# Kernel optimization log

Measured on AMD Instinct MI355X. Metric: run time of the kernel, lower is better.

Reference implementation:

```python
import jax, jax.numpy as jnp
import numpy as np

B, L, D, H = 2, 4096, 1024, 8
DK = D // H   # per-head key dim = 128
DV = D // H   # per-head value dim = 128
K_CONV = 4
CHUNK = 64
EPS = 1e-6


def _rmsnorm(x, w):
    return x * jax.lax.rsqrt(jnp.mean(x * x, axis=-1, keepdims=True) + EPS) * w


def _l2norm(x):
    return x * jax.lax.rsqrt(jnp.sum(x * x, axis=-1, keepdims=True) + EPS)


def _short_conv(x, w):
    # causal depthwise conv (FLA ShortConvolution) + silu. x: [B,L,C], w: [C,K]
    Kc = w.shape[-1]
    Ln = x.shape[1]
    xp = jnp.pad(x, ((0, 0), (Kc - 1, 0), (0, 0)))
    y = xp[:, 0:Ln, :] * w[:, 0]
    for i in range(1, Kc):
        y = y + xp[:, i:i + Ln, :] * w[:, i]
    return jax.nn.silu(y)


def _delta_chunkwise(q, k, v, beta, chunk=CHUNK):
    # q,k: [B,H,L,DK], v: [B,H,L,DV], beta: [B,H,L]
    Bb, Hh, Ll, Dk = q.shape
    Dv = v.shape[-1]
    q = q * (Dk ** -0.5)
    nC = Ll // chunk  # L divisible by chunk here, no padding needed
    qc = q.reshape(Bb, Hh, nC, chunk, Dk).transpose(2, 0, 1, 3, 4)
    kc = k.reshape(Bb, Hh, nC, chunk, Dk).transpose(2, 0, 1, 3, 4)
    vc = v.reshape(Bb, Hh, nC, chunk, Dv).transpose(2, 0, 1, 3, 4)
    bc = beta.reshape(Bb, Hh, nC, chunk).transpose(2, 0, 1, 3)
    eye = jnp.eye(chunk, dtype=q.dtype)
    causal = jnp.tril(jnp.ones((chunk, chunk), dtype=q.dtype))

    def step(S, inp):
        q_c, k_c, v_c, b_c = inp
        kk = jnp.einsum('bhik,bhjk->bhij', k_c, k_c)
        A = eye + jnp.tril(b_c[..., :, None] * kk, k=-1)
        A_inv = jax.lax.linalg.triangular_solve(
            A, jnp.broadcast_to(eye, A.shape), left_side=True, lower=True,
            transpose_a=False, conjugate_a=False, unit_diagonal=False)
        w_ = jnp.einsum('bhij,bhjk->bhik', A_inv, k_c * b_c[..., None])
        u_ = jnp.einsum('bhij,bhjv->bhiv', A_inv, v_c * b_c[..., None])
        v_new = u_ - jnp.einsum('bhik,bhkv->bhiv', w_, S)
        qk = jnp.einsum('bhik,bhjk->bhij', q_c, k_c)
        o = jnp.einsum('bhik,bhkv->bhiv', q_c, S) + jnp.einsum('bhij,bhjv->bhiv', qk * causal, v_new)
        S_new = S + jnp.einsum('bhik,bhiv->bhkv', k_c, v_new)
        return S_new, o

    S0 = jnp.zeros((Bb, Hh, Dk, Dv), dtype=q.dtype)
    S_f, outs = jax.lax.scan(step, S0, (qc, kc, vc, bc))
    out = outs.transpose(1, 2, 0, 3, 4).reshape(Bb, Hh, Ll, Dv)
    return out, S_f


def setup_inputs() -> dict:
    key = jax.random.key(0)
    ks = jax.random.split(key, 9)
    s = 0.02
    return {
        'x': jax.random.normal(ks[0], (B, L, D), jnp.float32),
        'norm_w': jnp.ones((D,), jnp.float32),
        'Wq': jax.random.normal(ks[1], (D, D), jnp.float32) * s,
        'Wk': jax.random.normal(ks[2], (D, D), jnp.float32) * s,
        'Wv': jax.random.normal(ks[3], (D, D), jnp.float32) * s,
        'Wb': jax.random.normal(ks[4], (D, H), jnp.float32) * s,
        'conv_q': jax.random.normal(ks[5], (D, K_CONV), jnp.float32) * 0.3,
        'conv_k': jax.random.normal(ks[6], (D, K_CONV), jnp.float32) * 0.3,
        'conv_v': jax.random.normal(ks[7], (D, K_CONV), jnp.float32) * 0.3,
        'o_norm_w': jnp.ones((DV,), jnp.float32),
        'Wo': jax.random.normal(ks[8], (D, D), jnp.float32) * s,
    }


def reference(x, norm_w, Wq, Wk, Wv, Wb, conv_q, conv_k, conv_v, o_norm_w, Wo):
    h = _rmsnorm(x, norm_w)
    q = _short_conv(h @ Wq, conv_q)
    k = _short_conv(h @ Wk, conv_k)
    v = _short_conv(h @ Wv, conv_v)
    beta = jax.nn.sigmoid(h @ Wb)                      # [B,L,H]
    qh = q.reshape(B, L, H, DK).transpose(0, 2, 1, 3)  # [B,H,L,DK]
    kh = k.reshape(B, L, H, DK).transpose(0, 2, 1, 3)
    vh = v.reshape(B, L, H, DV).transpose(0, 2, 1, 3)
    qh = _l2norm(jax.nn.silu(qh))  # qk_activation=silu, qk_norm=l2
    kh = _l2norm(jax.nn.silu(kh))
    bh = beta.transpose(0, 2, 1)   # [B,H,L]
    o, _ = _delta_chunkwise(qh, kh, vh, bh)
    o = o.transpose(0, 2, 1, 3)    # [B,L,H,DV]
    o = _rmsnorm(o, o_norm_w)      # per-head output RMSNorm
    return x + o.reshape(B, L, D) @ Wo
```

## Files before the change

kernel.cpp:

```cpp
#include <hip/hip_runtime.h>
#include <hip/hip_bf16.h>

#define B_ 2
#define L_ 4096
#define D_ 1024
#define H_ 8
#define DK_ 128
#define NR_ (B_*L_)
#define NC_ 64
#define CS_ 64

typedef __attribute__((ext_vector_type(8))) short short8;
typedef __attribute__((ext_vector_type(4))) float f32x4;

__device__ __forceinline__ float sigmf(float x){ return 1.0f/(1.0f+__expf(-x)); }
__device__ __forceinline__ float siluf(float x){ return x/(1.0f+__expf(-x)); }
__device__ __forceinline__ unsigned short f2bf(float f){
  __hip_bfloat16 h = __float2bfloat16(f);
  return *reinterpret_cast<unsigned short*>(&h);
}
__device__ __forceinline__ void gll16(const void* g, void* l){
  __builtin_amdgcn_global_load_lds((const __attribute__((address_space(1))) void*)g,
      (__attribute__((address_space(3))) void*)l, 16, 0, 0);
}

__global__ __launch_bounds__(256) void rmsnorm_kernel(const float* __restrict__ x,
    const float* __restrict__ w, float* __restrict__ h, unsigned short* __restrict__ hb){
  int n = blockIdx.x; int t = threadIdx.x;
  float4 v = ((const float4*)(x + (size_t)n*D_))[t];
  float ss = v.x*v.x + v.y*v.y + v.z*v.z + v.w*v.w;
  #pragma unroll
  for (int m=32;m>0;m>>=1) ss += __shfl_xor(ss, m, 64);
  __shared__ float red[4];
  if ((t&63)==0) red[t>>6] = ss;
  __syncthreads();
  ss = red[0]+red[1]+red[2]+red[3];
  float rs = rsqrtf(ss*(1.0f/D_) + 1e-6f);
  float4 wv = ((const float4*)w)[t];
  float4 o; o.x=v.x*rs*wv.x; o.y=v.y*rs*wv.y; o.z=v.z*rs*wv.z; o.w=v.w*rs*wv.w;
  ((float4*)(h + (size_t)n*D_))[t] = o;
  ushort4 ob4; ob4.x=f2bf(o.x); ob4.y=f2bf(o.y); ob4.z=f2bf(o.z); ob4.w=f2bf(o.w);
  ((ushort4*)(hb + (size_t)n*D_))[t] = ob4;
}

__global__ __launch_bounds__(256) void transpose_bf16_kernel(const float* __restrict__ W,
    unsigned short* __restrict__ Wt){
  __shared__ float tile[64][65];
  int bi = blockIdx.y, bj = blockIdx.x;
  int tx = threadIdx.x & 63, tg = threadIdx.x >> 6;
  #pragma unroll
  for (int i=0;i<16;i++){
    int r = tg*16 + i;
    tile[r][tx] = W[(size_t)(bi*64 + r)*D_ + bj*64 + tx];
  }
  __syncthreads();
  #pragma unroll
  for (int i=0;i<16;i++){
    int r = tg*16 + i;
    Wt[(size_t)(bj*64 + r)*D_ + bi*64 + tx] = f2bf(tile[tx][r]);
  }
}

__global__ __launch_bounds__(256) void gemm_bf16(const unsigned short* __restrict__ A,
    const unsigned short* __restrict__ Bt, const float* __restrict__ R,
    float* __restrict__ C, int N, int K){
  __shared__ __align__(16) unsigned short Al[4096];
  __shared__ __align__(16) unsigned short Bl[4096];
  int t = threadIdx.x, w = t>>6, l = t&63;
  int wm = w&1, wn = w>>1;
  int row0 = blockIdx.y*128, col0 = blockIdx.x*128;
  int lr = l&15, lk = l>>4;
  const unsigned short* ga0 = A  + (size_t)(row0 + w*16     + lr)*K + lk*8;
  const unsigned short* ga1 = A  + (size_t)(row0 + (w+4)*16 + lr)*K + lk*8;
  const unsigned short* gb0 = Bt + (size_t)(col0 + w*16     + lr)*K + lk*8;
  const unsigned short* gb1 = Bt + (size_t)(col0 + (w+4)*16 + lr)*K + lk*8;
  unsigned short* la0 = &Al[(w*64 + l)*8];
  unsigned short* la1 = &Al[((w+4)*64 + l)*8];
  unsigned short* lb0 = &Bl[(w*64 + l)*8];
  unsigned short* lb1 = &Bl[((w+4)*64 + l)*8];
  f32x4 acc[4][4];
  #pragma unroll
  for (int i=0;i<4;i++)
    #pragma unroll
    for (int j=0;j<4;j++) acc[i][j] = (f32x4){0.f,0.f,0.f,0.f};
  for (int k0=0;k0<K;k0+=32){
    gll16(ga0 + k0, la0);
    gll16(ga1 + k0, la1);
    gll16(gb0 + k0, lb0);
    gll16(gb1 + k0, lb1);
    __syncthreads();
    short8 af[4], bfr[4];
    #pragma unroll
    for (int i=0;i<4;i++) af[i]  = *(const short8*)&Al[((wm*4+i)*64 + l)*8];
    #pragma unroll
    for (int j=0;j<4;j++) bfr[j] = *(const short8*)&Bl[((wn*4+j)*64 + l)*8];
    #pragma unroll
    for (int i=0;i<4;i++)
      #pragma unroll
      for (int j=0;j<4;j++)
        acc[i][j] = __builtin_amdgcn_mfma_f32_16x16x32_bf16(af[i], bfr[j], acc[i][j], 0,0,0);
    __syncthreads();
  }
  int orow = row0 + wm*64 + (l>>4)*4;
  int ocol = col0 + wn*64 + (l&15);
  #pragma unroll
  for (int i=0;i<4;i++){
    #pragma unroll
    for (int j=0;j<4;j++){
      #pragma unroll
      for (int r=0;r<4;r++){
        size_t idx = (size_t)(orow + i*16 + r)*N + ocol + j*16;
        float res = R ? R[idx] : 0.0f;
        C[idx] = acc[i][j][r] + res;
      }
    }
  }
}

__global__ __launch_bounds__(256) void beta_kernel(const float* __restrict__ h,
    const float* __restrict__ Wb, float* __restrict__ beta){
  int n = blockIdx.x, t = threadIdx.x;
  const float* hr = h + (size_t)n*D_;
  float p[8] = {};
  for (int kx=t; kx<D_; kx+=256){
    float hv = hr[kx];
    const float* wr = Wb + (size_t)kx*H_;
    #pragma unroll
    for (int j=0;j<8;j++) p[j] += hv*wr[j];
  }
  #pragma unroll
  for (int m=32;m>0;m>>=1){
    #pragma unroll
    for (int j=0;j<8;j++) p[j] += __shfl_xor(p[j], m, 64);
  }
  __shared__ float red[4][8];
  if ((t&63)==0){
    #pragma unroll
    for (int j=0;j<8;j++) red[t>>6][j] = p[j];
  }
  __syncthreads();
  if (t < 8){
    float s = red[0][t]+red[1][t]+red[2][t]+red[3][t];
    beta[(size_t)n*H_ + t] = sigmf(s);
  }
}

__global__ __launch_bounds__(256) void conv_silu_kernel(const float* __restrict__ in,
    const float* __restrict__ w, float* __restrict__ out, int ld){
  size_t idx = (size_t)blockIdx.x*256 + threadIdx.x;
  int c = (int)(idx & (D_-1));
  int n = (int)(idx >> 10);
  int l = n & (L_-1);
  const float* src = in + (size_t)n*ld + c;
  float4 wv = ((const float4*)w)[c];
  float acc = wv.w * src[0];
  if (l >= 1) acc += wv.z * src[-ld];
  if (l >= 2) acc += wv.y * src[-2*ld];
  if (l >= 3) acc += wv.x * src[-3*ld];
  out[(size_t)n*D_ + c] = siluf(acc);
}

__global__ __launch_bounds__(256) void silu_l2norm_kernel(float* __restrict__ a, float scale,
    unsigned short* __restrict__ ob){
  int n = blockIdx.x, t = threadIdx.x;
  float* row = a + (size_t)n*D_;
  float4 v = ((const float4*)row)[t];
  float4 u; u.x=siluf(v.x); u.y=siluf(v.y); u.z=siluf(v.z); u.w=siluf(v.w);
  float ss = u.x*u.x+u.y*u.y+u.z*u.z+u.w*u.w;
  #pragma unroll
  for (int m=16;m>0;m>>=1) ss += __shfl_xor(ss, m, 64);
  float rs = rsqrtf(ss + 1e-6f) * scale;
  u.x*=rs; u.y*=rs; u.z*=rs; u.w*=rs;
  ((float4*)row)[t] = u;
  if (ob){
    ushort4 r4; r4.x=f2bf(u.x); r4.y=f2bf(u.y); r4.z=f2bf(u.z); r4.w=f2bf(u.w);
    ((ushort4*)(ob + (size_t)n*D_))[t] = r4;
  }
}

__global__ __launch_bounds__(256) void chunk_local_kernel(
    const float* __restrict__ q, const float* __restrict__ k, const float* __restrict__ v,
    const float* __restrict__ beta, unsigned short* __restrict__ wneg_buf,
    float* __restrict__ u_buf, unsigned short* __restrict__ qk_buf,
    unsigned short* __restrict__ kt_buf){
  int ci = blockIdx.x, bh = blockIdx.y;
  int b = bh >> 3, hh = bh & 7;
  int n0 = b*L_ + ci*CS_;
  int cbase = hh*DK_;
  int cid = bh*NC_ + ci;
  __shared__ float Ks[64][132];
  __shared__ float Als[64*68];
  __shared__ float rowW[144];
  __shared__ float rowU[144];
  __shared__ float bs[64];
  int t = threadIdx.x;
  {
    int r = t >> 2, c0 = (t & 3)*32;
    const float* kr = k + (size_t)(n0+r)*D_ + cbase + c0;
    #pragma unroll
    for (int m=0;m<32;m+=4) *(float4*)&Ks[r][c0+m] = *(const float4*)&kr[m];
  }
  if (t < 64) bs[t] = beta[(size_t)(n0+t)*H_ + hh];
  __syncthreads();
  int ti = t >> 4, tj = t & 15;
  {
    float cc[4][4] = {};
    #pragma unroll 2
    for (int d=0; d<128; d+=4){
      float4 ar[4], br[4];
      #pragma unroll
      for (int r2=0;r2<4;r2++) ar[r2] = *(const float4*)&Ks[ti+16*r2][d];
      #pragma unroll
      for (int s2=0;s2<4;s2++) br[s2] = *(const float4*)&Ks[tj+16*s2][d];
      #pragma unroll
      for (int r2=0;r2<4;r2++){
        #pragma unroll
        for (int s2=0;s2<4;s2++){
          cc[r2][s2] += ar[r2].x*br[s2].x + ar[r2].y*br[s2].y
                      + ar[r2].z*br[s2].z + ar[r2].w*br[s2].w;
        }
      }
    }
    #pragma unroll
    for (int r2=0;r2<4;r2++){
      #pragma unroll
      for (int s2=0;s2<4;s2++){
        int i2 = ti + 16*r2, j2 = tj + 16*s2;
        Als[i2*68 + j2] = (j2 < i2) ? bs[i2]*cc[r2][s2] : 0.0f;
      }
    }
  }
  __syncthreads();
  int i = t >> 2, part = t & 3, ds = part*32, dp = part*36;
  float wreg[32], ureg[32];
  {
    float bi = bs[i];
    const float* vr = v + (size_t)(n0+i)*D_ + cbase + ds;
    #pragma unroll
    for (int m=0;m<32;m++) wreg[m] = bi * Ks[i][ds+m];
    #pragma unroll
    for (int m=0;m<32;m+=4){
      float4 vv = *(const float4*)&vr[m];
      ureg[m+0]=bi*vv.x; ureg[m+1]=bi*vv.y; ureg[m+2]=bi*vv.z; ureg[m+3]=bi*vv.w;
    }
  }
  for (int j=0;j<63;j++){
    if (i == j){
      #pragma unroll
      for (int m=0;m<32;m++){ rowW[dp+m]=wreg[m]; rowU[dp+m]=ureg[m]; }
    }
    __syncthreads();
    if (i > j){
      float aj = Als[i*68 + j];
      #pragma unroll
      for (int m=0;m<32;m++){ wreg[m] -= aj*rowW[dp+m]; ureg[m] -= aj*rowU[dp+m]; }
    }
    __syncthreads();
  }
  {
    unsigned short* wd = wneg_buf + (size_t)cid*(64*128) + (size_t)i*128 + ds;
    float* ud = u_buf + (size_t)cid*(64*128) + (size_t)i*128 + ds;
    #pragma unroll
    for (int m=0;m<32;m+=4){
      ushort4 f; f.x=f2bf(-wreg[m]); f.y=f2bf(-wreg[m+1]); f.z=f2bf(-wreg[m+2]); f.w=f2bf(-wreg[m+3]);
      *(ushort4*)&wd[m] = f;
      float4 g; g.x=ureg[m]; g.y=ureg[m+1]; g.z=ureg[m+2]; g.w=ureg[m+3];
      *(float4*)&ud[m] = g;
    }
  }
  __syncthreads();
  {
    const float* qbase = q + (size_t)n0*D_ + cbase;
    float cc[4][4] = {};
    #pragma unroll 2
    for (int d=0; d<128; d+=4){
      float4 ar[4], br[4];
      #pragma unroll
      for (int r2=0;r2<4;r2++) ar[r2] = *(const float4*)&qbase[(size_t)(ti+16*r2)*D_ + d];
      #pragma unroll
      for (int s2=0;s2<4;s2++) br[s2] = *(const float4*)&Ks[tj+16*s2][d];
      #pragma unroll
      for (int r2=0;r2<4;r2++){
        #pragma unroll
        for (int s2=0;s2<4;s2++){
          cc[r2][s2] += ar[r2].x*br[s2].x + ar[r2].y*br[s2].y
                      + ar[r2].z*br[s2].z + ar[r2].w*br[s2].w;
        }
      }
    }
    unsigned short* qkd = qk_buf + (size_t)cid*4096;
    #pragma unroll
    for (int r2=0;r2<4;r2++){
      #pragma unroll
      for (int s2=0;s2<4;s2++){
        int i2 = ti+16*r2, j2 = tj+16*s2;
        qkd[i2*64 + j2] = (j2 <= i2) ? f2bf(cc[r2][s2]) : (unsigned short)0;
      }
    }
  }
  {
    unsigned short* ktd = kt_buf + (size_t)cid*(64*128);
    for (int idx = t; idx < 8192; idx += 256){
      int d = idx >> 6, i2 = idx & 63;
      ktd[idx] = f2bf(Ks[i2][d]);
    }
  }
}

__global__ __launch_bounds__(256) void seq_kernel(
    const unsigned short* __restrict__ wneg_buf, const float* __restrict__ u_buf,
    const unsigned short* __restrict__ kt_buf, const unsigned short* __restrict__ qk_buf,
    const unsigned short* __restrict__ qbh, float* __restrict__ o_buf){
  int bid = blockIdx.x;
  int bh = bid & 15, cg = bid >> 4;
  int b = bh >> 3, hh = bh & 7;
  int cbase = hh*DK_;
  int t = threadIdx.x;
  int wv = t >> 6, l = t & 63, g = l >> 4, lr = l & 15;

  __shared__ __align__(16) unsigned short Wl[2][8192];
  __shared__ __align__(16) unsigned short Ql[2][8192];
  __shared__ __align__(16) unsigned short Ktl[2][8192];
  __shared__ __align__(16) unsigned short qkl[2][4096];
  __shared__ __align__(16) float  Ul[2][2048];
  __shared__ __align__(16) unsigned short Stl[32*136];
  __shared__ __align__(16) unsigned short vTl[32*72];

  f32x4 Sacc[2][2];
  #pragma unroll
  for (int mc=0;mc<2;mc++)
    #pragma unroll
    for (int ntl=0;ntl<2;ntl++) Sacc[mc][ntl] = (f32x4){0.f,0.f,0.f,0.f};

  for (int z=t; z<32*136; z+=256) Stl[z] = 0;
  __syncthreads();

  size_t cid0 = (size_t)bh*NC_;
  const unsigned short* wb_  = wneg_buf + cid0*8192;
  const unsigned short* ktb_ = kt_buf  + cid0*8192;
  const unsigned short* qkb_ = qk_buf  + cid0*4096;
  const float*          ub_  = u_buf   + cid0*8192;
  const unsigned short* qb_  = qbh + (size_t)(b*L_)*D_ + cbase;

  int hv = wv >> 1, lv = wv & 1;

  #define STAGE(BI, CI) do { \
    const unsigned short* wp  = wb_  + (size_t)(CI)*8192; \
    const unsigned short* kp  = ktb_ + (size_t)(CI)*8192; \
    const unsigned short* qkp = qkb_ + (size_t)(CI)*4096; \
    const float*          up  = ub_  + (size_t)(CI)*8192; \
    const unsigned short* qp  = qb_  + (size_t)(CI)*CS_*D_; \
    _Pragma("unroll") \
    for (int r=0;r<4;r++){ \
      gll16(wp + (size_t)(16*r + lr)*128 + wv*32 + g*8, &Wl[BI][(r*4+wv)*512 + l*8]); \
      gll16(qp + (size_t)(16*r + lr)*D_  + wv*32 + g*8, &Ql[BI][(r*4+wv)*512 + l*8]); \
      int fn = 2*r + hv; \
      gll16(kp + (size_t)(16*fn + lr)*64 + lv*32 + g*8, &Ktl[BI][(r*4+wv)*512 + l*8]); \
    } \
    _Pragma("unroll") \
    for (int r=0;r<2;r++){ \
      int fm = 2*r + hv; \
      gll16(qkp + (size_t)(16*fm + lr)*64 + lv*32 + g*8, &qkl[BI][(r*4+wv)*512 + l*8]); \
      int idx = r*256 + t; \
      gll16(up + (size_t)(idx>>3)*128 + cg*32 + (idx&7)*4, &Ul[BI][idx*4]); \
    } \
  } while(0)

  STAGE(0, 0);
  asm volatile("s_waitcnt vmcnt(0)" ::: "memory");
  __builtin_amdgcn_s_barrier();
  __builtin_amdgcn_sched_barrier(0);

  int cur = 0;
  for (int ci=0; ci<NC_; ++ci){
    int cn = (ci+1 < NC_) ? ci+1 : ci;
    STAGE(cur^1, cn);

    f32x4 accV[2];
    #pragma unroll
    for (int nt=0;nt<2;nt++){
      #pragma unroll
      for (int r=0;r<4;r++) accV[nt][r] = Ul[cur][(16*wv + 4*g + r)*32 + 16*nt + lr];
    }
    #pragma unroll
    for (int kq=0;kq<4;kq++){
      short8 a  = *(const short8*)&Wl[cur][(wv*4+kq)*512 + l*8];
      short8 b0 = *(const short8*)&Stl[(0  + lr)*136 + kq*32 + g*8];
      short8 b1 = *(const short8*)&Stl[(16 + lr)*136 + kq*32 + g*8];
      accV[0] = __builtin_amdgcn_mfma_f32_16x16x32_bf16(a, b0, accV[0], 0,0,0);
      accV[1] = __builtin_amdgcn_mfma_f32_16x16x32_bf16(a, b1, accV[1], 0,0,0);
    }
    #pragma unroll
    for (int nt=0;nt<2;nt++){
      #pragma unroll
      for (int r=0;r<4;r++)
        vTl[(16*nt + lr)*72 + 16*wv + 4*g + r] = f2bf(accV[nt][r]);
    }
    asm volatile("s_waitcnt lgkmcnt(0)" ::: "memory");
    __builtin_amdgcn_s_barrier();
    __builtin_amdgcn_sched_barrier(0);

    f32x4 accO[2];
    accO[0] = (f32x4){0.f,0.f,0.f,0.f}; accO[1] = (f32x4){0.f,0.f,0.f,0.f};
    #pragma unroll
    for (int kq=0;kq<4;kq++){
      short8 a  = *(const short8*)&Ql[cur][(wv*4+kq)*512 + l*8];
      short8 b0 = *(const short8*)&Stl[(0  + lr)*136 + kq*32 + g*8];
      short8 b1 = *(const short8*)&Stl[(16 + lr)*136 + kq*32 + g*8];
      accO[0] = __builtin_amdgcn_mfma_f32_16x16x32_bf16(a, b0, accO[0], 0,0,0);
      accO[1] = __builtin_amdgcn_mfma_f32_16x16x32_bf16(a, b1, accO[1], 0,0,0);
    }
    #pragma unroll
    for (int kq=0;kq<2;kq++){
      short8 a  = *(const short8*)&qkl[cur][(wv*2+kq)*512 + l*8];
      short8 b0 = *(const short8*)&vTl[(0  + lr)*72 + kq*32 + g*8];
      short8 b1 = *(const short8*)&vTl[(16 + lr)*72 + kq*32 + g*8];
      accO[0] = __builtin_amdgcn_mfma_f32_16x16x32_bf16(a, b0, accO[0], 0,0,0);
      accO[1] = __builtin_amdgcn_mfma_f32_16x16x32_bf16(a, b1, accO[1], 0,0,0);
    }
    {
      int n0 = b*L_ + ci*CS_;
      #pragma unroll
      for (int nt=0;nt<2;nt++){
        #pragma unroll
        for (int r=0;r<4;r++)
          o_buf[(size_t)(n0 + 16*wv + 4*g + r)*D_ + cbase + cg*32 + 16*nt + lr] = accO[nt][r];
      }
    }
    asm volatile("s_waitcnt lgkmcnt(0)" ::: "memory");
    __builtin_amdgcn_s_barrier();
    __builtin_amdgcn_sched_barrier(0);

    #pragma unroll
    for (int kq=0;kq<2;kq++){
      short8 a0 = *(const short8*)&vTl[(0  + lr)*72 + kq*32 + g*8];
      short8 a1 = *(const short8*)&vTl[(16 + lr)*72 + kq*32 + g*8];
      short8 b0 = *(const short8*)&Ktl[cur][((2*wv+0)*2 + kq)*512 + l*8];
      short8 b1 = *(const short8*)&Ktl[cur][((2*wv+1)*2 + kq)*512 + l*8];
      Sacc[0][0] = __builtin_amdgcn_mfma_f32_16x16x32_bf16(a0, b0, Sacc[0][0], 0,0,0);
      Sacc[0][1] = __builtin_amdgcn_mfma_f32_16x16x32_bf16(a0, b1, Sacc[0][1], 0,0,0);
      Sacc[1][0] = __builtin_amdgcn_mfma_f32_16x16x32_bf16(a1, b0, Sacc[1][0], 0,0,0);
      Sacc[1][1] = __builtin_amdgcn_mfma_f32_16x16x32_bf16(a1, b1, Sacc[1][1], 0,0,0);
    }
    #pragma unroll
    for (int mc=0;mc<2;mc++){
      #pragma unroll
      for (int ntl=0;ntl<2;ntl++){
        #pragma unroll
        for (int r=0;r<4;r++)
          Stl[(16*mc + 4*g + r)*136 + 32*wv + 16*ntl + lr] = f2bf(Sacc[mc][ntl][r]);
      }
    }
    asm volatile("s_waitcnt lgkmcnt(0)" ::: "memory");
    asm volatile("s_waitcnt vmcnt(4)" ::: "memory");
    __builtin_amdgcn_s_barrier();
    __builtin_amdgcn_sched_barrier(0);
    cur ^= 1;
  }
  #undef STAGE
}

__global__ __launch_bounds__(256) void head_rmsnorm_kernel(const float* __restrict__ o,
    const float* __restrict__ w, unsigned short* __restrict__ out){
  int n = blockIdx.x, t = threadIdx.x;
  float4 v = ((const float4*)(o + (size_t)n*D_))[t];
  float ss = v.x*v.x+v.y*v.y+v.z*v.z+v.w*v.w;
  #pragma unroll
  for (int m=16;m>0;m>>=1) ss += __shfl_xor(ss, m, 64);
  float rs = rsqrtf(ss*(1.0f/DK_) + 1e-6f);
  float4 wv = ((const float4*)w)[t & 31];
  float4 u; u.x=v.x*rs*wv.x; u.y=v.y*rs*wv.y; u.z=v.z*rs*wv.z; u.w=v.w*rs*wv.w;
  ushort4 r4; r4.x=f2bf(u.x); r4.y=f2bf(u.y); r4.z=f2bf(u.z); r4.w=f2bf(u.w);
  ((ushort4*)(out + (size_t)n*D_))[t] = r4;
}

extern "C" void kernel_launch(void* const* d_in, const int* in_sizes, int n_in,
                              void* d_out, int out_size, void* d_ws, size_t ws_size,
                              hipStream_t stream){
  const float* x      = (const float*)d_in[0];
  const float* norm_w = (const float*)d_in[1];
  const float* Wq     = (const float*)d_in[2];
  const float* Wk     = (const float*)d_in[3];
  const float* Wv     = (const float*)d_in[4];
  const float* Wb     = (const float*)d_in[5];
  const float* conv_q = (const float*)d_in[6];
  const float* conv_k = (const float*)d_in[7];
  const float* conv_v = (const float*)d_in[8];
  const float* onw    = (const float*)d_in[9];
  const float* Wo     = (const float*)d_in[10];
  float* out = (float*)d_out;

  const size_t NB = (size_t)NR_*D_;
  float* ws   = (float*)d_ws;
  float* h    = ws;
  float* qkv  = ws + NB;
  float* qb   = ws + 4*NB;
  float* kb   = ws + 5*NB;
  float* vb   = ws + 6*NB;
  float* betab= ws + 7*NB;
  unsigned short* wtq = (unsigned short*)(betab + 65536);
  unsigned short* wtk = wtq + (size_t)D_*D_;
  unsigned short* wtv = wtk + (size_t)D_*D_;
  unsigned short* wto = wtv + (size_t)D_*D_;
  unsigned short* hb  = (unsigned short*)qb;
  unsigned short* obb = (unsigned short*)h;
  unsigned short* wneg = (unsigned short*)qkv;
  unsigned short* ktb  = wneg + (size_t)8*1024*1024;
  unsigned short* qkbf = ktb  + (size_t)8*1024*1024;
  unsigned short* qbh  = qkbf + (size_t)4*1024*1024;
  float*          ubuf = (float*)(qbh + (size_t)8*1024*1024);

  rmsnorm_kernel<<<NR_, 256, 0, stream>>>(x, norm_w, h, hb);
  dim3 tg(16,16);
  transpose_bf16_kernel<<<tg, 256, 0, stream>>>(Wq, wtq);
  transpose_bf16_kernel<<<tg, 256, 0, stream>>>(Wk, wtk);
  transpose_bf16_kernel<<<tg, 256, 0, stream>>>(Wv, wtv);
  transpose_bf16_kernel<<<tg, 256, 0, stream>>>(Wo, wto);
  dim3 gq(3*D_/128, NR_/128);
  gemm_bf16<<<gq, 256, 0, stream>>>(hb, wtq, nullptr, qkv, 3*D_, D_);
  beta_kernel<<<NR_, 256, 0, stream>>>(h, Wb, betab);
  conv_silu_kernel<<<(int)(NB/256), 256, 0, stream>>>(qkv,        conv_q, qb, 3*D_);
  conv_silu_kernel<<<(int)(NB/256), 256, 0, stream>>>(qkv + D_,   conv_k, kb, 3*D_);
  conv_silu_kernel<<<(int)(NB/256), 256, 0, stream>>>(qkv + 2*D_, conv_v, vb, 3*D_);
  const float qscale = 0.08838834764831845f;
  silu_l2norm_kernel<<<NR_, 256, 0, stream>>>(qb, qscale, qbh);
  silu_l2norm_kernel<<<NR_, 256, 0, stream>>>(kb, 1.0f, nullptr);
  chunk_local_kernel<<<dim3(NC_, 16), 256, 0, stream>>>(qb, kb, vb, betab,
      wneg, ubuf, qkbf, ktb);
  seq_kernel<<<64, 256, 0, stream>>>(wneg, ubuf, ktb, qkbf, qbh, vb);
  head_rmsnorm_kernel<<<NR_, 256, 0, stream>>>(vb, onw, obb);
  dim3 gg(D_/128, NR_/128);
  gemm_bf16<<<gg, 256, 0, stream>>>(obb, wto, x, out, D_, D_);
  (void)in_sizes; (void)n_in; (void)out_size; (void)ws_size;
}
```

Before: 744.2 us.

## Fuse conv+silu+l2norm for q/k and restructure seq kernel to 512 threads

Merges the causal depthwise conv+silu with the silu+l2norm pass for q and k into one row kernel, so the intermediate q/k buffers are not written and reread. The sequential chunk kernel goes from 256 to 512 threads, with each wave owning one 16x16 output tile. The state update is overlapped with the output computation by double-buffering the bf16 state in LDS, which removes one barrier per chunk. The bf16 q buffer is moved into a workspace region no longer in use, and the layout of the staged loads is recomputed once up front.

New measurement: 688.6 us. 7.5% less time.

```diff
diff --git a/kernel.cpp b/kernel.cpp
--- a/kernel.cpp
+++ b/kernel.cpp
@@ -160,18 +160,33 @@
   out[(size_t)n*D_ + c] = siluf(acc);
 }
 
-__global__ __launch_bounds__(256) void silu_l2norm_kernel(float* __restrict__ a, float scale,
-    unsigned short* __restrict__ ob){
+__global__ __launch_bounds__(256) void conv_silu_l2norm_kernel(const float* __restrict__ in,
+    const float* __restrict__ w, float* __restrict__ outf, unsigned short* __restrict__ ob,
+    float scale, int ld){
   int n = blockIdx.x, t = threadIdx.x;
-  float* row = a + (size_t)n*D_;
-  float4 v = ((const float4*)row)[t];
-  float4 u; u.x=siluf(v.x); u.y=siluf(v.y); u.z=siluf(v.z); u.w=siluf(v.w);
+  int c0 = t*4;
+  int l = n & (L_-1);
+  const float* src = in + (size_t)n*ld + c0;
+  float4 x0 = *(const float4*)&src[0];
+  float4 x1 = (l>=1) ? *(const float4*)&src[-ld]   : (float4){0,0,0,0};
+  float4 x2 = (l>=2) ? *(const float4*)&src[-2*ld] : (float4){0,0,0,0};
+  float4 x3 = (l>=3) ? *(const float4*)&src[-3*ld] : (float4){0,0,0,0};
+  float4 w0 = ((const float4*)w)[c0+0];
+  float4 w1 = ((const float4*)w)[c0+1];
+  float4 w2 = ((const float4*)w)[c0+2];
+  float4 w3 = ((const float4*)w)[c0+3];
+  float4 u;
+  u.x = siluf(w0.w*x0.x + w0.z*x1.x + w0.y*x2.x + w0.x*x3.x);
+  u.y = siluf(w1.w*x0.y + w1.z*x1.y + w1.y*x2.y + w1.x*x3.y);
+  u.z = siluf(w2.w*x0.z + w2.z*x1.z + w2.y*x2.z + w2.x*x3.z);
+  u.w = siluf(w3.w*x0.w + w3.z*x1.w + w3.y*x2.w + w3.x*x3.w);
+  u.x = siluf(u.x); u.y = siluf(u.y); u.z = siluf(u.z); u.w = siluf(u.w);
   float ss = u.x*u.x+u.y*u.y+u.z*u.z+u.w*u.w;
   #pragma unroll
   for (int m=16;m>0;m>>=1) ss += __shfl_xor(ss, m, 64);
   float rs = rsqrtf(ss + 1e-6f) * scale;
   u.x*=rs; u.y*=rs; u.z*=rs; u.w*=rs;
-  ((float4*)row)[t] = u;
+  ((float4*)(outf + (size_t)n*D_))[t] = u;
   if (ob){
     ushort4 r4; r4.x=f2bf(u.x); r4.y=f2bf(u.y); r4.z=f2bf(u.z); r4.w=f2bf(u.w);
     ((ushort4*)(ob + (size_t)n*D_))[t] = r4;
@@ -307,7 +322,7 @@
   }
 }
 
-__global__ __launch_bounds__(256) void seq_kernel(
+__global__ __launch_bounds__(512) void seq_kernel(
     const unsigned short* __restrict__ wneg_buf, const float* __restrict__ u_buf,
     const unsigned short* __restrict__ kt_buf, const unsigned short* __restrict__ qk_buf,
     const unsigned short* __restrict__ qbh, float* __restrict__ o_buf){
@@ -316,24 +331,23 @@
   int b = bh >> 3, hh = bh & 7;
   int cbase = hh*DK_;
   int t = threadIdx.x;
-  int wv = t >> 6, l = t & 63, g = l >> 4, lr = l & 15;
+  int w = t >> 6, l = t & 63, g = l >> 4, lr = l & 15;
+  int mt = w >> 1, nt = w & 1;
+  int ct = w >> 2, dtp = (w & 3)*2;
 
   __shared__ __align__(16) unsigned short Wl[2][8192];
   __shared__ __align__(16) unsigned short Ql[2][8192];
   __shared__ __align__(16) unsigned short Ktl[2][8192];
   __shared__ __align__(16) unsigned short qkl[2][4096];
   __shared__ __align__(16) float  Ul[2][2048];
-  __shared__ __align__(16) unsigned short Stl[32*136];
+  __shared__ __align__(16) unsigned short Stl[2][32*136];
   __shared__ __align__(16) unsigned short vTl[32*72];
 
-  f32x4 Sacc[2][2];
-  #pragma unroll
-  for (int mc=0;mc<2;mc++)
-    #pragma unroll
-    for (int ntl=0;ntl<2;ntl++) Sacc[mc][ntl] = (f32x4){0.f,0.f,0.f,0.f};
-
-  for (int z=t; z<32*136; z+=256) Stl[z] = 0;
-  __syncthreads();
+  f32x4 Sacc[2];
+  Sacc[0] = (f32x4){0.f,0.f,0.f,0.f};
+  Sacc[1] = (f32x4){0.f,0.f,0.f,0.f};
+
+  for (int z=t; z<2*32*136; z+=512) ((unsigned short*)Stl)[z] = 0;
 
   size_t cid0 = (size_t)bh*NC_;
   const unsigned short* wb_  = wneg_buf + cid0*8192;
@@ -342,7 +356,23 @@
   const float*          ub_  = u_buf   + cid0*8192;
   const unsigned short* qb_  = qbh + (size_t)(b*L_)*D_ + cbase;
 
-  int hv = wv >> 1, lv = wv & 1;
+  int offW[2], offQ[2], offK[2];
+  #pragma unroll
+  for (int r=0;r<2;r++){
+    int u = r*512 + t;
+    int fm = u>>8, kq = (u>>6)&3, ll = u&63;
+    offW[r] = (16*fm + (ll&15))*128 + kq*32 + (ll>>4)*8;
+    offQ[r] = (16*fm + (ll&15))*D_  + kq*32 + (ll>>4)*8;
+    int fn = u>>7, kqk = (u>>6)&1;
+    offK[r] = (16*fn + (ll&15))*64 + kqk*32 + (ll>>4)*8;
+  }
+  int offQk, offU;
+  {
+    int u = t;
+    int fm = u>>7, kq = (u>>6)&1, ll = u&63;
+    offQk = (16*fm + (ll&15))*64 + kq*32 + (ll>>4)*8;
+    offU  = (u>>3)*128 + cg*32 + (u&7)*4;
+  }
 
   #define STAGE(BI, CI) do { \
     const unsigned short* wp  = wb_  + (size_t)(CI)*8192; \
@@ -351,23 +381,17 @@
     const float*          up  = ub_  + (size_t)(CI)*8192; \
     const unsigned short* qp  = qb_  + (size_t)(CI)*CS_*D_; \
     _Pragma("unroll") \
-    for (int r=0;r<4;r++){ \
-      gll16(wp + (size_t)(16*r + lr)*128 + wv*32 + g*8, &Wl[BI][(r*4+wv)*512 + l*8]); \
-      gll16(qp + (size_t)(16*r + lr)*D_  + wv*32 + g*8, &Ql[BI][(r*4+wv)*512 + l*8]); \
-      int fn = 2*r + hv; \
-      gll16(kp + (size_t)(16*fn + lr)*64 + lv*32 + g*8, &Ktl[BI][(r*4+wv)*512 + l*8]); \
+    for (int r=0;r<2;r++){ \
+      gll16(wp + offW[r], &Wl[BI][(r*512+t)*8]); \
+      gll16(qp + offQ[r], &Ql[BI][(r*512+t)*8]); \
+      gll16(kp + offK[r], &Ktl[BI][(r*512+t)*8]); \
     } \
-    _Pragma("unroll") \
-    for (int r=0;r<2;r++){ \
-      int fm = 2*r + hv; \
-      gll16(qkp + (size_t)(16*fm + lr)*64 + lv*32 + g*8, &qkl[BI][(r*4+wv)*512 + l*8]); \
-      int idx = r*256 + t; \
-      gll16(up + (size_t)(idx>>3)*128 + cg*32 + (idx&7)*4, &Ul[BI][idx*4]); \
-    } \
+    gll16(qkp + offQk, &qkl[BI][t*8]); \
+    gll16(up + offU, &Ul[BI][t*4]); \
   } while(0)
 
   STAGE(0, 0);
-  asm volatile("s_waitcnt vmcnt(0)" ::: "memory");
+  asm volatile("s_waitcnt vmcnt(0) lgkmcnt(0)" ::: "memory");
   __builtin_amdgcn_s_barrier();
   __builtin_amdgcn_sched_barrier(0);
 
@@ -376,80 +400,54 @@
     int cn = (ci+1 < NC_) ? ci+1 : ci;
     STAGE(cur^1, cn);
 
-    f32x4 accV[2];
-    #pragma unroll
-    for (int nt=0;nt<2;nt++){
-      #pragma unroll
-      for (int r=0;r<4;r++) accV[nt][r] = Ul[cur][(16*wv + 4*g + r)*32 + 16*nt + lr];
-    }
+    f32x4 accV;
+    #pragma unroll
+    for (int r=0;r<4;r++) accV[r] = Ul[cur][(16*mt + 4*g + r)*32 + 16*nt + lr];
     #pragma unroll
     for (int kq=0;kq<4;kq++){
-      short8 a  = *(const short8*)&Wl[cur][(wv*4+kq)*512 + l*8];
-      short8 b0 = *(const short8*)&Stl[(0  + lr)*136 + kq*32 + g*8];
-      short8 b1 = *(const short8*)&Stl[(16 + lr)*136 + kq*32 + g*8];
-      accV[0] = __builtin_amdgcn_mfma_f32_16x16x32_bf16(a, b0, accV[0], 0,0,0);
-      accV[1] = __builtin_amdgcn_mfma_f32_16x16x32_bf16(a, b1, accV[1], 0,0,0);
-    }
-    #pragma unroll
-    for (int nt=0;nt<2;nt++){
-      #pragma unroll
-      for (int r=0;r<4;r++)
-        vTl[(16*nt + lr)*72 + 16*wv + 4*g + r] = f2bf(accV[nt][r]);
-    }
+      short8 a  = *(const short8*)&Wl[cur][(mt*4+kq)*512 + l*8];
+      short8 b0 = *(const short8*)&Stl[cur][(16*nt + lr)*136 + kq*32 + g*8];
+      accV = __builtin_amdgcn_mfma_f32_16x16x32_bf16(a, b0, accV, 0,0,0);
+    }
+    #pragma unroll
+    for (int r=0;r<4;r++)
+      vTl[(16*nt + lr)*72 + 16*mt + 4*g + r] = f2bf(accV[r]);
     asm volatile("s_waitcnt lgkmcnt(0)" ::: "memory");
     __builtin_amdgcn_s_barrier();
     __builtin_amdgcn_sched_barrier(0);
 
-    f32x4 accO[2];
-    accO[0] = (f32x4){0.f,0.f,0.f,0.f}; accO[1] = (f32x4){0.f,0.f,0.f,0.f};
+    #pragma unroll
+    for (int kq=0;kq<2;kq++){
+      short8 aD = *(const short8*)&vTl[(16*ct + lr)*72 + kq*32 + g*8];
+      short8 bD0 = *(const short8*)&Ktl[cur][((dtp+0)*2 + kq)*512 + l*8];
+      short8 bD1 = *(const short8*)&Ktl[cur][((dtp+1)*2 + kq)*512 + l*8];
+      Sacc[0] = __builtin_amdgcn_mfma_f32_16x16x32_bf16(aD, bD0, Sacc[0], 0,0,0);
+      Sacc[1] = __builtin_amdgcn_mfma_f32_16x16x32_bf16(aD, bD1, Sacc[1], 0,0,0);
+    }
+    f32x4 accO = (f32x4){0.f,0.f,0.f,0.f};
     #pragma unroll
     for (int kq=0;kq<4;kq++){
-      short8 a  = *(const short8*)&Ql[cur][(wv*4+kq)*512 + l*8];
-      short8 b0 = *(const short8*)&Stl[(0  + lr)*136 + kq*32 + g*8];
-      short8 b1 = *(const short8*)&Stl[(16 + lr)*136 + kq*32 + g*8];
-      accO[0] = __builtin_amdgcn_mfma_f32_16x16x32_bf16(a, b0, accO[0], 0,0,0);
-      accO[1] = __builtin_amdgcn_mfma_f32_16x16x32_bf16(a, b1, accO[1], 0,0,0);
+      short8 a  = *(const short8*)&Ql[cur][(mt*4+kq)*512 + l*8];
+      short8 b0 = *(const short8*)&Stl[cur][(16*nt + lr)*136 + kq*32 + g*8];
+      accO = __builtin_amdgcn_mfma_f32_16x16x32_bf16(a, b0, accO, 0,0,0);
     }
     #pragma unroll
     for (int kq=0;kq<2;kq++){
-      short8 a  = *(const short8*)&qkl[cur][(wv*2+kq)*512 + l*8];
-      short8 b0 = *(const short8*)&vTl[(0  + lr)*72 + kq*32 + g*8];
-      short8 b1 = *(const short8*)&vTl[(16 + lr)*72 + kq*32 + g*8];
-      accO[0] = __builtin_amdgcn_mfma_f32_16x16x32_bf16(a, b0, accO[0], 0,0,0);
-      accO[1] = __builtin_amdgcn_mfma_f32_16x16x32_bf16(a, b1, accO[1], 0,0,0);
+      short8 a  = *(const short8*)&qkl[cur][(mt*2+kq)*512 + l*8];
+      short8 b0 = *(const short8*)&vTl[(16*nt + lr)*72 + kq*32 + g*8];
+      accO = __builtin_amdgcn_mfma_f32_16x16x32_bf16(a, b0, accO, 0,0,0);
+    }
+    #pragma unroll
+    for (int j=0;j<2;j++){
+      #pragma unroll
+      for (int r=0;r<4;r++)
+        Stl[cur^1][(16*ct + 4*g + r)*136 + 16*(dtp+j) + lr] = f2bf(Sacc[j][r]);
     }
     {
       int n0 = b*L_ + ci*CS_;
       #pragma unroll
-      for (int nt=0;nt<2;nt++){
-        #pragma unroll
-        for (int r=0;r<4;r++)
-          o_buf[(size_t)(n0 + 16*wv + 4*g + r)*D_ + cbase + cg*32 + 16*nt + lr] = accO[nt][r];
-      }
-    }
-    asm volatile("s_waitcnt lgkmcnt(0)" ::: "memory");
-    __builtin_amdgcn_s_barrier();
-    __builtin_amdgcn_sched_barrier(0);
-
-    #pragma unroll
-    for (int kq=0;kq<2;kq++){
-      short8 a0 = *(const short8*)&vTl[(0  + lr)*72 + kq*32 + g*8];
-      short8 a1 = *(const short8*)&vTl[(16 + lr)*72 + kq*32 + g*8];
-      short8 b0 = *(const short8*)&Ktl[cur][((2*wv+0)*2 + kq)*512 + l*8];
-      short8 b1 = *(const short8*)&Ktl[cur][((2*wv+1)*2 + kq)*512 + l*8];
-      Sacc[0][0] = __builtin_amdgcn_mfma_f32_16x16x32_bf16(a0, b0, Sacc[0][0], 0,0,0);
-      Sacc[0][1] = __builtin_amdgcn_mfma_f32_16x16x32_bf16(a0, b1, Sacc[0][1], 0,0,0);
-      Sacc[1][0] = __builtin_amdgcn_mfma_f32_16x16x32_bf16(a1, b0, Sacc[1][0], 0,0,0);
-      Sacc[1][1] = __builtin_amdgcn_mfma_f32_16x16x32_bf16(a1, b1, Sacc[1][1], 0,0,0);
-    }
-    #pragma unroll
-    for (int mc=0;mc<2;mc++){
-      #pragma unroll
-      for (int ntl=0;ntl<2;ntl++){
-        #pragma unroll
-        for (int r=0;r<4;r++)
-          Stl[(16*mc + 4*g + r)*136 + 32*wv + 16*ntl + lr] = f2bf(Sacc[mc][ntl][r]);
-      }
+      for (int r=0;r<4;r++)
+        o_buf[(size_t)(n0 + 16*mt + 4*g + r)*D_ + cbase + cg*32 + 16*nt + lr] = accO[r];
     }
     asm volatile("s_waitcnt lgkmcnt(0)" ::: "memory");
     asm volatile("s_waitcnt vmcnt(4)" ::: "memory");
@@ -504,11 +502,11 @@
   unsigned short* wto = wtv + (size_t)D_*D_;
   unsigned short* hb  = (unsigned short*)qb;
   unsigned short* obb = (unsigned short*)h;
+  unsigned short* qbh = (unsigned short*)(h + NB/2);
   unsigned short* wneg = (unsigned short*)qkv;
   unsigned short* ktb  = wneg + (size_t)8*1024*1024;
   unsigned short* qkbf = ktb  + (size_t)8*1024*1024;
-  unsigned short* qbh  = qkbf + (size_t)4*1024*1024;
-  float*          ubuf = (float*)(qbh + (size_t)8*1024*1024);
+  float*          ubuf = (float*)(qkbf + (size_t)4*1024*1024);
 
   rmsnorm_kernel<<<NR_, 256, 0, stream>>>(x, norm_w, h, hb);
   dim3 tg(16,16);
@@ -519,15 +517,13 @@
   dim3 gq(3*D_/128, NR_/128);
   gemm_bf16<<<gq, 256, 0, stream>>>(hb, wtq, nullptr, qkv, 3*D_, D_);
   beta_kernel<<<NR_, 256, 0, stream>>>(h, Wb, betab);
-  conv_silu_kernel<<<(int)(NB/256), 256, 0, stream>>>(qkv,        conv_q, qb, 3*D_);
-  conv_silu_kernel<<<(int)(NB/256), 256, 0, stream>>>(qkv + D_,   conv_k, kb, 3*D_);
+  const float qscale = 0.08838834764831845f;
+  conv_silu_l2norm_kernel<<<NR_, 256, 0, stream>>>(qkv,      conv_q, qb, qbh, qscale, 3*D_);
+  conv_silu_l2norm_kernel<<<NR_, 256, 0, stream>>>(qkv + D_, conv_k, kb, nullptr, 1.0f, 3*D_);
   conv_silu_kernel<<<(int)(NB/256), 256, 0, stream>>>(qkv + 2*D_, conv_v, vb, 3*D_);
-  const float qscale = 0.08838834764831845f;
-  silu_l2norm_kernel<<<NR_, 256, 0, stream>>>(qb, qscale, qbh);
-  silu_l2norm_kernel<<<NR_, 256, 0, stream>>>(kb, 1.0f, nullptr);
   chunk_local_kernel<<<dim3(NC_, 16), 256, 0, stream>>>(qb, kb, vb, betab,
       wneg, ubuf, qkbf, ktb);
-  seq_kernel<<<64, 256, 0, stream>>>(wneg, ubuf, ktb, qkbf, qbh, vb);
+  seq_kernel<<<64, 512, 0, stream>>>(wneg, ubuf, ktb, qkbf, qbh, vb);
   head_rmsnorm_kernel<<<NR_, 256, 0, stream>>>(vb, onw, obb);
   dim3 gg(D_/128, NR_/128);
   gemm_bf16<<<gg, 256, 0, stream>>>(obb, wto, x, out, D_, D_);
```
